# Kernel optimization log

Measured on AMD Instinct MI355X. Metric: run time of the kernel, lower is better.

Reference implementation:

```python
import jax, jax.numpy as jnp
import numpy as np

B, C, T = 32, 273, 4096
CHOUT = 270
N_SUBJECTS = 200
POS_DIM = 256
MARGIN = 0.2
INVALID = -0.1
N_FREQS = int((POS_DIM // 2) ** 0.5)          # 11
ACTUAL_POS_DIM = N_FREQS * N_FREQS * 2        # 242
NEG_INF = -1e9  # exp(-1e9)==0 in fp32, identical softmax to -inf but grad-safe


def fourier_emb(positions):
    # positions: [..., 2] -> [..., 2*n_freqs^2]
    freqs = jnp.arange(N_FREQS, dtype=positions.dtype)
    width = 1.0 + 2.0 * MARGIN
    p = positions + MARGIN
    scale = 2.0 * np.pi / width
    # loc[..., i, j] = x * f_i * scale + y * f_j * scale
    loc = (p[..., 0, None, None] * (scale * freqs[:, None])
           + p[..., 1, None, None] * (scale * freqs[None, :]))
    loc = loc.reshape(*positions.shape[:-1], N_FREQS * N_FREQS)
    return jnp.concatenate([jnp.cos(loc), jnp.sin(loc)], axis=-1)


def setup_inputs() -> dict:
    key = jax.random.key(0)
    k1, k2, k3, k4 = jax.random.split(key, 4)
    meg = jax.random.normal(k1, (B, C, T), dtype=jnp.float32)
    positions = jax.random.uniform(k2, (B, C, 2), dtype=jnp.float32)
    # last 16 channels per sample are invalid (sentinel -0.1 on both coords)
    positions = positions.at[:, -16:, :].set(INVALID)
    subject_index = jax.random.randint(k3, (B,), 0, N_SUBJECTS)
    heads = jax.random.normal(k4, (N_SUBJECTS, CHOUT, ACTUAL_POS_DIM),
                              dtype=jnp.float32) / np.sqrt(ACTUAL_POS_DIM)
    return {"meg": meg, "positions": positions,
            "subject_index": subject_index, "heads": heads}


def reference(meg, positions, subject_index, heads):
    # meg: [B,C,T], positions: [B,C,2], subject_index: [B],
    # heads: [n_subjects, chout, pos_dim]
    embedding = fourier_emb(positions)                       # [B,C,D]
    invalid = jnp.all(positions == INVALID, axis=-1)         # [B,C]
    score_offset = jnp.where(invalid, NEG_INF, 0.0).astype(meg.dtype)
    h = heads[subject_index]                                 # [B,chout,D] per-subject gather
    scores = jnp.einsum('bcd,bod->boc', embedding, h) + score_offset[:, None, :]
    weights = jax.nn.softmax(scores, axis=2)                 # softmax over channels
    out = jnp.einsum('bct,boc->bot', meg, weights)           # [B,chout,T]
    return out
```

## Files before the change

### kernel.cpp

```cpp
#include <hip/hip_runtime.h>

#define NB 32
#define NC 273
#define NT 4096
#define NO 270
#define ND 242
#define OPAD 288
#define CPAD 288
#define TBLK 64

typedef __attribute__((ext_vector_type(8))) short short8;
typedef __attribute__((ext_vector_type(4))) float f32x4;

__device__ __forceinline__ short f2bf(float f) {
    union { float f; unsigned int u; } x;
    x.f = f;
    unsigned int r = x.u + 0x7fffu + ((x.u >> 16) & 1u);
    return (short)(r >> 16);
}

__global__ void emb_kernel(const float* __restrict__ pos, float* __restrict__ emb) {
    const int g = blockIdx.x * 256 + threadIdx.x;
    const int TOT = NB * NC * 121;
    if (g >= TOT) return;
    const int p = g / 121;
    const int idx = g - p * 121;
    const int fi = idx / 11;
    const int fj = idx - fi * 11;
    const float scale = 4.487989505128276f;
    const float px = pos[p * 2] + 0.2f;
    const float py = pos[p * 2 + 1] + 0.2f;
    const float loc = px * (scale * (float)fi) + py * (scale * (float)fj);
    emb[(size_t)p * ND + idx] = cosf(loc);
    emb[(size_t)p * ND + 121 + idx] = sinf(loc);
}

__global__ __launch_bounds__(256) void scores_kernel(
    const float* __restrict__ emb, const float* __restrict__ heads,
    const int* __restrict__ subj, const float* __restrict__ pos,
    float* __restrict__ scores) {
    __shared__ float As[16 * 36];
    __shared__ float Bs[16 * 68];
    const int b = blockIdx.z;
    const int o0 = blockIdx.y * 32;
    const int c0 = blockIdx.x * 64;
    const int tid = threadIdx.x;
    const int s = subj[b];
    const int tx = tid & 15, ty = tid >> 4;
    const int srow = tid >> 3;
    const int sfp = tid & 7;

    float acc[2][4] = {};

    for (int kc = 0; kc < 256; kc += 16) {
        const int d = kc + sfp * 2;
        {
            const int o = o0 + srow;
            float2 av = make_float2(0.f, 0.f);
            if (d < ND && o < NO)
                av = *reinterpret_cast<const float2*>(
                    &heads[((size_t)(s * NO + o)) * ND + d]);
            As[(sfp * 2 + 0) * 36 + srow] = av.x;
            As[(sfp * 2 + 1) * 36 + srow] = av.y;
        }
#pragma unroll
        for (int half = 0; half < 2; ++half) {
            const int row = srow + half * 32;
            const int c = c0 + row;
            float2 bv = make_float2(0.f, 0.f);
            if (d < ND && c < NC)
                bv = *reinterpret_cast<const float2*>(
                    &emb[((size_t)(b * NC + c)) * ND + d]);
            Bs[(sfp * 2 + 0) * 68 + row] = bv.x;
            Bs[(sfp * 2 + 1) * 68 + row] = bv.y;
        }
        __syncthreads();
#pragma unroll
        for (int k = 0; k < 16; ++k) {
            const float2 a = *reinterpret_cast<const float2*>(&As[k * 36 + ty * 2]);
            const float4 bvv = *reinterpret_cast<const float4*>(&Bs[k * 68 + tx * 4]);
            const float aa[2] = {a.x, a.y};
            const float bb[4] = {bvv.x, bvv.y, bvv.z, bvv.w};
#pragma unroll
            for (int ii = 0; ii < 2; ++ii)
#pragma unroll
                for (int jj = 0; jj < 4; ++jj) acc[ii][jj] += aa[ii] * bb[jj];
        }
        __syncthreads();
    }

#pragma unroll
    for (int ii = 0; ii < 2; ++ii) {
        const int o = o0 + ty * 2 + ii;
        if (o >= NO) continue;
#pragma unroll
        for (int jj = 0; jj < 4; ++jj) {
            const int c = c0 + tx * 4 + jj;
            if (c >= NC) continue;
            const float px = pos[((size_t)(b * NC + c)) * 2];
            const float py = pos[((size_t)(b * NC + c)) * 2 + 1];
            const float off = (px == -0.1f && py == -0.1f) ? -1e9f : 0.0f;
            scores[((size_t)(b * NO + o)) * NC + c] = acc[ii][jj] + off;
        }
    }
}

__global__ __launch_bounds__(64) void softmax_kernel(
    const float* __restrict__ scores, short* __restrict__ wbf) {
    const int row = blockIdx.x;
    const int b = row / OPAD;
    const int o = row - b * OPAD;
    short* w = wbf + (size_t)row * CPAD;
    const int lane = threadIdx.x;

    if (o >= NO) {
        for (int c = lane; c < CPAD; c += 64) w[c] = 0;
        return;
    }

    const float* s = scores + ((size_t)(b * NO + o)) * NC;
    float v[5];
    int cnt = 0;
    float mx = -1e30f;
    for (int c = lane; c < NC; c += 64) {
        v[cnt] = s[c];
        mx = fmaxf(mx, v[cnt]);
        ++cnt;
    }
#pragma unroll
    for (int off = 32; off; off >>= 1) mx = fmaxf(mx, __shfl_xor(mx, off));
    float sum = 0.0f;
    for (int i = 0; i < cnt; ++i) {
        v[i] = expf(v[i] - mx);
        sum += v[i];
    }
#pragma unroll
    for (int off = 32; off; off >>= 1) sum += __shfl_xor(sum, off);
    const float inv = 1.0f / sum;
    int i = 0;
    for (int c = lane; c < CPAD; c += 64) {
        float val = 0.0f;
        if (c < NC) val = v[i++] * inv;
        w[c] = f2bf(val);
    }
}

__global__ __launch_bounds__(256) void einsum_kernel(
    const float* __restrict__ meg, const short* __restrict__ wbf,
    float* __restrict__ out) {
    __shared__ short Alds[OPAD * 40];
    const int b = blockIdx.z;
    const int t0 = blockIdx.x * TBLK;
    const int tid = threadIdx.x;
    const int l = tid & 63;
    const int wv = tid >> 6;
    const int mw = wv >> 1;
    const int tw = wv & 1;
    const int q = l >> 4;
    const int nlo = l & 15;

    f32x4 acc[9][2];
#pragma unroll
    for (int i = 0; i < 9; ++i)
#pragma unroll
        for (int j = 0; j < 2; ++j) acc[i][j] = {0.f, 0.f, 0.f, 0.f};

    const float* mbase = meg + ((size_t)b * NC) * NT + t0 + tw * 32 + nlo;
    const short* wbase = wbf + ((size_t)b * OPAD) * CPAD;

    for (int kc = 0; kc < CPAD; kc += 32) {
        float bf0[8], bf1[8];
#pragma unroll
        for (int j = 0; j < 8; ++j) {
            int c = kc + q * 8 + j;
            if (c >= NC) c = 0;
            const float* mrow = mbase + (size_t)c * NT;
            bf0[j] = mrow[0];
            bf1[j] = mrow[16];
        }
        for (int sidx = tid; sidx < OPAD * 4; sidx += 256) {
            const int row = sidx >> 2;
            const int q4 = sidx & 3;
            const short8 v = *reinterpret_cast<const short8*>(
                wbase + (size_t)row * CPAD + kc + q4 * 8);
            *reinterpret_cast<short8*>(&Alds[row * 40 + q4 * 8]) = v;
        }
        __syncthreads();
        short8 b0, b1;
#pragma unroll
        for (int j = 0; j < 8; ++j) {
            b0[j] = f2bf(bf0[j]);
            b1[j] = f2bf(bf1[j]);
        }
#pragma unroll
        for (int mt = 0; mt < 9; ++mt) {
            const short8 av = *reinterpret_cast<const short8*>(
                &Alds[(mw * 144 + mt * 16 + nlo) * 40 + q * 8]);
            acc[mt][0] = __builtin_amdgcn_mfma_f32_16x16x32_bf16(av, b0, acc[mt][0], 0, 0, 0);
            acc[mt][1] = __builtin_amdgcn_mfma_f32_16x16x32_bf16(av, b1, acc[mt][1], 0, 0, 0);
        }
        __syncthreads();
    }

    const int tcol = t0 + tw * 32 + nlo;
#pragma unroll
    for (int mt = 0; mt < 9; ++mt) {
        const int ob = mw * 144 + mt * 16 + q * 4;
#pragma unroll
        for (int nf = 0; nf < 2; ++nf) {
            const int t = tcol + nf * 16;
#pragma unroll
            for (int r = 0; r < 4; ++r) {
                const int o = ob + r;
                if (o < NO) out[((size_t)(b * NO + o)) * NT + t] = acc[mt][nf][r];
            }
        }
    }
}

extern "C" void kernel_launch(void* const* d_in, const int* in_sizes, int n_in,
                              void* d_out, int out_size, void* d_ws, size_t ws_size,
                              hipStream_t stream) {
    const float* meg = (const float*)d_in[0];
    const float* pos = (const float*)d_in[1];
    const int* subj = (const int*)d_in[2];
    const float* heads = (const float*)d_in[3];
    float* out = (float*)d_out;

    float* emb = (float*)d_ws;
    float* scores = emb + (size_t)NB * NC * ND;
    short* wbf = (short*)(scores + (size_t)NB * NO * NC);

    const int emb_items = NB * NC * 121;
    emb_kernel<<<dim3((emb_items + 255) / 256), dim3(256), 0, stream>>>(pos, emb);
    scores_kernel<<<dim3(5, 9, NB), dim3(256), 0, stream>>>(emb, heads, subj, pos, scores);
    softmax_kernel<<<dim3(NB * OPAD), dim3(64), 0, stream>>>(scores, wbf);
    einsum_kernel<<<dim3(NT / TBLK, 1, NB), dim3(256), 0, stream>>>(meg, wbf, out);
}
```

Before: 376.9 us.

## Software-pipeline einsum K loop with register-prefetched meg and wider LDS stages

Restructures the einsum kernel's channel loop into three stages of 96 channels each. The next stage's meg values are prefetched into registers while the current stage's MFMAs run, and each stage stages three 32-channel weight slices into a larger shared buffer. The aim is to hide global load latency and cut the number of barriers. In exchange it uses many more registers (96 floats of prefetch per thread) and a larger LDS footprint (about 69KB), which can lower occupancy.

```diff
diff --git a/kernel.cpp b/kernel.cpp
--- a/kernel.cpp
+++ b/kernel.cpp
@@ -148,7 +148,7 @@
 __global__ __launch_bounds__(256) void einsum_kernel(
     const float* __restrict__ meg, const short* __restrict__ wbf,
     float* __restrict__ out) {
-    __shared__ short Alds[OPAD * 40];
+    __shared__ short Alds[3 * 288 * 40];
     const int b = blockIdx.z;
     const int t0 = blockIdx.x * TBLK;
     const int tid = threadIdx.x;
@@ -168,39 +168,66 @@
     const float* mbase = meg + ((size_t)b * NC) * NT + t0 + tw * 32 + nlo;
     const short* wbase = wbf + ((size_t)b * OPAD) * CPAD;
 
-    for (int kc = 0; kc < CPAD; kc += 32) {
-        float bf0[8], bf1[8];
-#pragma unroll
-        for (int j = 0; j < 8; ++j) {
-            int c = kc + q * 8 + j;
-            if (c >= NC) c = 0;
-            const float* mrow = mbase + (size_t)c * NT;
-            bf0[j] = mrow[0];
-            bf1[j] = mrow[16];
-        }
-        for (int sidx = tid; sidx < OPAD * 4; sidx += 256) {
-            const int row = sidx >> 2;
-            const int q4 = sidx & 3;
+    float Breg[2][3][8][2];
+
+    auto loadB = [&](int buf, int it) {
+#pragma unroll
+        for (int sub = 0; sub < 3; ++sub)
+#pragma unroll
+            for (int j = 0; j < 8; ++j) {
+                int c = it * 96 + sub * 32 + q * 8 + j;
+                if (c >= NC) c = 0;
+                const float* mrow = mbase + (size_t)c * NT;
+                Breg[buf][sub][j][0] = mrow[0];
+                Breg[buf][sub][j][1] = mrow[16];
+            }
+    };
+
+    auto stageA = [&](int it) {
+        for (int sidx = tid; sidx < 288 * 12; sidx += 256) {
+            const int sub = sidx / 1152;
+            const int r = sidx - sub * 1152;
+            const int row = r >> 2;
+            const int q4 = r & 3;
             const short8 v = *reinterpret_cast<const short8*>(
-                wbase + (size_t)row * CPAD + kc + q4 * 8);
-            *reinterpret_cast<short8*>(&Alds[row * 40 + q4 * 8]) = v;
-        }
-        __syncthreads();
-        short8 b0, b1;
-#pragma unroll
-        for (int j = 0; j < 8; ++j) {
-            b0[j] = f2bf(bf0[j]);
-            b1[j] = f2bf(bf1[j]);
-        }
-#pragma unroll
-        for (int mt = 0; mt < 9; ++mt) {
-            const short8 av = *reinterpret_cast<const short8*>(
-                &Alds[(mw * 144 + mt * 16 + nlo) * 40 + q * 8]);
-            acc[mt][0] = __builtin_amdgcn_mfma_f32_16x16x32_bf16(av, b0, acc[mt][0], 0, 0, 0);
-            acc[mt][1] = __builtin_amdgcn_mfma_f32_16x16x32_bf16(av, b1, acc[mt][1], 0, 0, 0);
-        }
-        __syncthreads();
-    }
+                wbase + (size_t)row * CPAD + it * 96 + sub * 32 + q4 * 8);
+            *reinterpret_cast<short8*>(&Alds[(sub * 288 + row) * 40 + q4 * 8]) = v;
+        }
+    };
+
+    auto mma = [&](int buf) {
+#pragma unroll
+        for (int sub = 0; sub < 3; ++sub) {
+            short8 b0, b1;
+#pragma unroll
+            for (int j = 0; j < 8; ++j) {
+                b0[j] = f2bf(Breg[buf][sub][j][0]);
+                b1[j] = f2bf(Breg[buf][sub][j][1]);
+            }
+#pragma unroll
+            for (int mt = 0; mt < 9; ++mt) {
+                const short8 av = *reinterpret_cast<const short8*>(
+                    &Alds[((sub * 288) + mw * 144 + mt * 16 + nlo) * 40 + q * 8]);
+                acc[mt][0] = __builtin_amdgcn_mfma_f32_16x16x32_bf16(av, b0, acc[mt][0], 0, 0, 0);
+                acc[mt][1] = __builtin_amdgcn_mfma_f32_16x16x32_bf16(av, b1, acc[mt][1], 0, 0, 0);
+            }
+        }
+    };
+
+    loadB(0, 0);
+    stageA(0);
+    __syncthreads();
+    loadB(1, 1);
+    mma(0);
+    __syncthreads();
+    stageA(1);
+    __syncthreads();
+    loadB(0, 2);
+    mma(1);
+    __syncthreads();
+    stageA(2);
+    __syncthreads();
+    mma(0);
 
     const int tcol = t0 + tw * 32 + nlo;
 #pragma unroll
```

New measurement: 372.7 us. Within noise of the previous version (-1.1%).

## Stage full weight tile in LDS once and prefetch meg in 3-deep register ring

Applied to the files above, without the earlier changes.

The einsum kernel now loads the whole bf16 weight matrix for a batch (all 9 channel chunks, padded to 272 rows) into LDS once, in MFMA-fragment order, and drops the per-chunk sync pairs. Each wave covers all 17 output tiles for its own 32 time columns, so the time block doubles to 128 and each meg element is read once per block. A three-slot register ring prefetches meg rows three chunks ahead to overlap global loads with MFMA work. The cost is about 157KB of LDS per block, launch bounds pinned to one block per CU, and many more accumulator registers, which lowers occupancy.

```diff
diff --git a/kernel.cpp b/kernel.cpp
--- a/kernel.cpp
+++ b/kernel.cpp
@@ -5,9 +5,10 @@
 #define NT 4096
 #define NO 270
 #define ND 242
-#define OPAD 288
+#define OPAD 272
 #define CPAD 288
-#define TBLK 64
+#define TBLK 128
+#define NMT 17
 
 typedef __attribute__((ext_vector_type(8))) short short8;
 typedef __attribute__((ext_vector_type(4))) float f32x4;
@@ -145,67 +146,80 @@
     }
 }
 
-__global__ __launch_bounds__(256) void einsum_kernel(
+__global__ __launch_bounds__(256, 1) void einsum_kernel(
     const float* __restrict__ meg, const short* __restrict__ wbf,
     float* __restrict__ out) {
-    __shared__ short Alds[OPAD * 40];
+    __shared__ short Alds[9 * NMT * 64 * 8];
     const int b = blockIdx.z;
     const int t0 = blockIdx.x * TBLK;
     const int tid = threadIdx.x;
     const int l = tid & 63;
-    const int wv = tid >> 6;
-    const int mw = wv >> 1;
-    const int tw = wv & 1;
+    const int tw = tid >> 6;
     const int q = l >> 4;
     const int nlo = l & 15;
 
-    f32x4 acc[9][2];
-#pragma unroll
-    for (int i = 0; i < 9; ++i)
+    f32x4 acc[NMT][2];
+#pragma unroll
+    for (int i = 0; i < NMT; ++i)
 #pragma unroll
         for (int j = 0; j < 2; ++j) acc[i][j] = {0.f, 0.f, 0.f, 0.f};
 
     const float* mbase = meg + ((size_t)b * NC) * NT + t0 + tw * 32 + nlo;
     const short* wbase = wbf + ((size_t)b * OPAD) * CPAD;
 
-    for (int kc = 0; kc < CPAD; kc += 32) {
-        float bf0[8], bf1[8];
+    float Breg[3][8][2];
+
+    auto loadB = [&](int slot, int ch) {
 #pragma unroll
         for (int j = 0; j < 8; ++j) {
-            int c = kc + q * 8 + j;
+            int c = ch * 32 + q * 8 + j;
             if (c >= NC) c = 0;
             const float* mrow = mbase + (size_t)c * NT;
-            bf0[j] = mrow[0];
-            bf1[j] = mrow[16];
-        }
-        for (int sidx = tid; sidx < OPAD * 4; sidx += 256) {
-            const int row = sidx >> 2;
-            const int q4 = sidx & 3;
-            const short8 v = *reinterpret_cast<const short8*>(
-                wbase + (size_t)row * CPAD + kc + q4 * 8);
-            *reinterpret_cast<short8*>(&Alds[row * 40 + q4 * 8]) = v;
-        }
-        __syncthreads();
+            Breg[slot][j][0] = mrow[0];
+            Breg[slot][j][1] = mrow[16];
+        }
+    };
+
+    loadB(0, 0);
+    loadB(1, 1);
+    loadB(2, 2);
+
+    for (int sidx = tid; sidx < 9 * NMT * 64; sidx += 256) {
+        const int ch = sidx / (NMT * 64);
+        const int rem = sidx - ch * (NMT * 64);
+        const int mt = rem >> 6;
+        const int ll = rem & 63;
+        const int row = mt * 16 + (ll & 15);
+        const int k = ch * 32 + (ll >> 4) * 8;
+        const short8 v = *reinterpret_cast<const short8*>(
+            wbase + (size_t)row * CPAD + k);
+        *reinterpret_cast<short8*>(&Alds[sidx * 8]) = v;
+    }
+    __syncthreads();
+
+#pragma unroll
+    for (int ch = 0; ch < 9; ++ch) {
+        const int slot = ch % 3;
         short8 b0, b1;
 #pragma unroll
         for (int j = 0; j < 8; ++j) {
-            b0[j] = f2bf(bf0[j]);
-            b1[j] = f2bf(bf1[j]);
-        }
-#pragma unroll
-        for (int mt = 0; mt < 9; ++mt) {
+            b0[j] = f2bf(Breg[slot][j][0]);
+            b1[j] = f2bf(Breg[slot][j][1]);
+        }
+        if (ch + 3 < 9) loadB(slot, ch + 3);
+#pragma unroll
+        for (int mt = 0; mt < NMT; ++mt) {
             const short8 av = *reinterpret_cast<const short8*>(
-                &Alds[(mw * 144 + mt * 16 + nlo) * 40 + q * 8]);
+                &Alds[((ch * NMT + mt) * 64 + l) * 8]);
             acc[mt][0] = __builtin_amdgcn_mfma_f32_16x16x32_bf16(av, b0, acc[mt][0], 0, 0, 0);
             acc[mt][1] = __builtin_amdgcn_mfma_f32_16x16x32_bf16(av, b1, acc[mt][1], 0, 0, 0);
         }
-        __syncthreads();
     }
 
     const int tcol = t0 + tw * 32 + nlo;
 #pragma unroll
-    for (int mt = 0; mt < 9; ++mt) {
-        const int ob = mw * 144 + mt * 16 + q * 4;
+    for (int mt = 0; mt < NMT; ++mt) {
+        const int ob = mt * 16 + q * 4;
 #pragma unroll
         for (int nf = 0; nf < 2; ++nf) {
             const int t = tcol + nf * 16;
```

Measured after the change: 370.2 us. Within noise of the previous version (-1.8%).
